# Kernel tuning notes

Hardware: AMD Instinct MI355X
Metric: run time of the kernel (lower is better)

Reference implementation:

```python
import jax, jax.numpy as jnp
import numpy as np

N_EMBED = 1024
N_HEADS = 16
HEAD_DIM = N_EMBED // N_HEADS


def setup_inputs() -> dict:
    key = jax.random.key(0)
    ks = jax.random.split(key, 5)
    x = jax.random.normal(ks[0], (4, 2048, N_EMBED), dtype=jnp.float32)
    # Linear params stored as [in, out] (y = x @ W + b), math-equivalent to torch Linear
    scale_attn = 1.0 / np.sqrt(N_EMBED)
    W_attn = jax.random.normal(ks[1], (N_EMBED, 3 * N_EMBED), dtype=jnp.float32) * scale_attn
    b_attn = jax.random.normal(ks[2], (3 * N_EMBED,), dtype=jnp.float32) * 0.02
    W_proj = jax.random.normal(ks[3], (N_EMBED, N_EMBED), dtype=jnp.float32) * scale_attn
    b_proj = jax.random.normal(ks[4], (N_EMBED,), dtype=jnp.float32) * 0.02
    return {"x": x, "W_attn": W_attn, "b_attn": b_attn, "W_proj": W_proj, "b_proj": b_proj}


def reference(x, W_attn, b_attn, W_proj, b_proj):
    BS, SL, ED = x.shape
    qkv = x @ W_attn + b_attn                      # [B, S, 3E]
    q, k, v = jnp.split(qkv, 3, axis=2)
    # [B, H, S, D]
    def heads(t):
        return t.reshape(BS, SL, N_HEADS, HEAD_DIM).transpose(0, 2, 1, 3)
    q, k, v = heads(q), heads(k), heads(v)
    att = jnp.einsum('bhqd,bhkd->bhqk', q, k) * (HEAD_DIM ** -0.5)
    causal = jnp.tril(jnp.ones((SL, SL), dtype=bool))
    att = jnp.where(causal[None, None], att, -jnp.inf)
    att = jax.nn.softmax(att, axis=-1)
    y = jnp.einsum('bhqk,bhkd->bhqd', att, v)      # [B, H, S, D]
    y = y.transpose(0, 2, 1, 3).reshape(BS, SL, ED)
    return y @ W_proj + b_proj
```

## Files before the change

### kernel.cpp

```cpp
#include <hip/hip_runtime.h>


#define BATCH 4
#define SEQ   2048
#define EMB   1024
#define NH    16
#define HD    64

typedef __bf16 bf16;
typedef __bf16 bf16x8 __attribute__((ext_vector_type(8)));
typedef float  f32x4  __attribute__((ext_vector_type(4)));

__device__ __forceinline__ void ld_lds16(const void* g, void* l) {
  __builtin_amdgcn_global_load_lds(
      (const __attribute__((address_space(1))) void*)g,
      (__attribute__((address_space(3))) void*)l, 16, 0, 0);
}

__global__ void cvt_f32_bf16(const float* __restrict__ in, bf16* __restrict__ out, int n) {
  int i = (blockIdx.x * blockDim.x + threadIdx.x) * 4;
  if (i + 3 < n) {
    float4 v = *(const float4*)(in + i);
    bf16 o0 = (bf16)v.x, o1 = (bf16)v.y, o2 = (bf16)v.z, o3 = (bf16)v.w;
    out[i] = o0; out[i+1] = o1; out[i+2] = o2; out[i+3] = o3;
  }
}

__global__ void transpose_cvt2(const float* __restrict__ Wa, const float* __restrict__ Wp,
                               bf16* __restrict__ WaT, bf16* __restrict__ WpT) {
  __shared__ float tile[32][33];
  int bx = blockIdx.x;
  const float* W; bf16* WT; int N;
  if (bx < 96) { W = Wa; WT = WaT; N = 3072; }
  else         { W = Wp; WT = WpT; N = 1024; bx -= 96; }
  int n0 = bx * 32, k0 = blockIdx.y * 32;
  int tx = threadIdx.x & 31, ty = threadIdx.x >> 5;
#pragma unroll
  for (int r = 0; r < 4; r++) {
    int k = k0 + ty + r * 8;
    tile[ty + r * 8][tx] = W[(long)k * N + n0 + tx];
  }
  __syncthreads();
#pragma unroll
  for (int r = 0; r < 4; r++) {
    int n = n0 + ty + r * 8;
    WT[(long)n * EMB + k0 + tx] = (bf16)tile[tx][ty + r * 8];
  }
}

#define QSCALE 0.18033688f

template <int BNT>
__global__ __launch_bounds__(256, 3) void gemm_bt(
    const bf16* __restrict__ A, const bf16* __restrict__ Bt,
    const float* __restrict__ bias, int Kdim, int Ncols, int mode,
    bf16* __restrict__ q, bf16* __restrict__ k, bf16* __restrict__ v,
    float* __restrict__ out)
{
  constexpr int NF = BNT / 32;
  __shared__ __align__(16) bf16 Al[128 * 64];
  __shared__ __align__(16) bf16 Bl[BNT * 64];
  int lin = blockIdx.x;
  int xcd = lin & 7, s = lin >> 3;
  int bx = s >> 3, by = xcd * 8 + (s & 7);
  int m0 = by * 128;
  int n0 = bx * BNT;
  int t = threadIdx.x;
  int wave = t >> 6, lane = t & 63;
  int l15 = lane & 15, quad = lane >> 4;
  int wm = (wave & 1) * 64, wn = (wave >> 1) * (BNT / 2);

  f32x4 acc[4][NF] = {};

  for (int kt = 0; kt < Kdim; kt += 64) {
    __syncthreads();
#pragma unroll
    for (int it = 0; it < 4; ++it) {
      int c = it * 256 + t;
      int row = c >> 3, u = c & 7;
      ld_lds16(&A[(long)(m0 + row) * Kdim + kt + ((u ^ (row & 7)) * 8)],
               &Al[(it * 256 + wave * 64) * 8]);
    }
#pragma unroll
    for (int it = 0; it < BNT / 32; ++it) {
      int c = it * 256 + t;
      int row = c >> 3, u = c & 7;
      ld_lds16(&Bt[(long)(n0 + row) * Kdim + kt + ((u ^ (row & 7)) * 8)],
               &Bl[(it * 256 + wave * 64) * 8]);
    }
    __syncthreads();
#pragma unroll
    for (int ks = 0; ks < 2; ++ks) {
      bf16x8 af[4], bfr[NF];
#pragma unroll
      for (int i = 0; i < 4; ++i) {
        int r = wm + i * 16 + l15;
        af[i] = *(const bf16x8*)(&Al[r * 64 + (((ks * 4 + quad) ^ (r & 7)) * 8)]);
      }
#pragma unroll
      for (int i = 0; i < NF; ++i) {
        int r = wn + i * 16 + l15;
        bfr[i] = *(const bf16x8*)(&Bl[r * 64 + (((ks * 4 + quad) ^ (r & 7)) * 8)]);
      }
#pragma unroll
      for (int mi = 0; mi < 4; ++mi)
#pragma unroll
        for (int ni = 0; ni < NF; ++ni)
          acc[mi][ni] = __builtin_amdgcn_mfma_f32_16x16x32_bf16(af[mi], bfr[ni], acc[mi][ni], 0, 0, 0);
    }
  }

#pragma unroll
  for (int mi = 0; mi < 4; ++mi) {
#pragma unroll
    for (int ni = 0; ni < NF; ++ni) {
      int gcol = n0 + wn + ni * 16 + l15;
      float bv = bias[gcol];
#pragma unroll
      for (int i = 0; i < 4; ++i) {
        int grow = m0 + wm + mi * 16 + quad * 4 + i;
        float val = acc[mi][ni][i] + bv;
        if (mode == 0) {
          int which = gcol >> 10, e = gcol & 1023;
          int h = e >> 6, d = e & 63;
          int b = grow >> 11, ss = grow & 2047;
          if (which == 0) {
            q[(((long)b * NH + h) * SEQ + ss) * HD + d] = (bf16)(val * QSCALE);
          } else if (which == 1) {
            k[(((long)b * NH + h) * SEQ + ss) * HD + d] = (bf16)val;
          } else {
            v[(((long)b * NH + h) * HD + d) * SEQ + ss] = (bf16)val;
          }
        } else {
          out[(long)grow * Ncols + gcol] = val;
        }
      }
    }
  }
}

#define LDP 72

__global__ __launch_bounds__(256, 2) void attn(
    const bf16* __restrict__ Q, const bf16* __restrict__ K,
    const bf16* __restrict__ Vt, bf16* __restrict__ Y)
{
  __shared__ __align__(16) bf16 Kl[64 * 64];
  __shared__ __align__(16) bf16 Vl[64 * 64];
  __shared__ __align__(16) bf16 Pl[4][32 * LDP];
  int L = blockIdx.x;
  int a = L >> 3;
  int hd = (L & 7) + 8 * (a & 7);
  int st = a >> 3;
  int b = hd >> 4, h = hd & 15;
  const bf16* Qp  = Q  + (((long)b * NH + h) * SEQ) * HD;
  const bf16* Kp  = K  + (((long)b * NH + h) * SEQ) * HD;
  const bf16* Vtp = Vt + (((long)b * NH + h) * HD) * SEQ;
  int t = threadIdx.x, wave = t >> 6, lane = t & 63;
  int l15 = lane & 15, quad = lane >> 4;

#pragma unroll 1
  for (int pass = 0; pass < 2; ++pass) {
    int q0 = (pass == 0) ? st * 128 : (SEQ - 128) - st * 128;
    int wq0 = q0 + wave * 32;

    bf16x8 qf[2][2];
#pragma unroll
    for (int m = 0; m < 2; ++m) {
      const bf16* qrow = Qp + (long)(wq0 + m * 16 + l15) * HD + quad * 8;
      qf[m][0] = *(const bf16x8*)(qrow);
      qf[m][1] = *(const bf16x8*)(qrow + 32);
    }
    float lrow[2][4] = {};
    f32x4 oacc[2][4] = {};

    int ntiles = q0 / 64 + 2;
#pragma unroll 1
    for (int kt = 0; kt < ntiles; ++kt) {
      int k0 = kt * 64;
      __syncthreads();
#pragma unroll
      for (int it = 0; it < 2; ++it) {
        int cu = it * 256 + t;
        int row = cu >> 3, u = cu & 7;
        ld_lds16(&Kp[(long)(k0 + row) * HD + ((u ^ (row & 7)) * 8)],
                 &Kl[(it * 256 + wave * 64) * 8]);
        ld_lds16(&Vtp[(long)row * SEQ + k0 + ((u ^ (row & 7)) * 8)],
                 &Vl[(it * 256 + wave * 64) * 8]);
      }
      __syncthreads();
      if (k0 > wq0 + 31) continue;

      f32x4 sc[2][4] = {};
#pragma unroll
      for (int kk = 0; kk < 2; ++kk) {
#pragma unroll
        for (int ni = 0; ni < 4; ++ni) {
          int r = ni * 16 + l15, u = kk * 4 + quad;
          bf16x8 kfr = *(const bf16x8*)(&Kl[r * 64 + ((u ^ (r & 7)) * 8)]);
          sc[0][ni] = __builtin_amdgcn_mfma_f32_16x16x32_bf16(qf[0][kk], kfr, sc[0][ni], 0, 0, 0);
          sc[1][ni] = __builtin_amdgcn_mfma_f32_16x16x32_bf16(qf[1][kk], kfr, sc[1][ni], 0, 0, 0);
        }
      }

      bool full = (k0 + 63 <= wq0);
#pragma unroll
      for (int m = 0; m < 2; ++m) {
#pragma unroll
        for (int i = 0; i < 4; ++i) {
          int qr = wq0 + m * 16 + quad * 4 + i;
          float e[4];
#pragma unroll
          for (int ni = 0; ni < 4; ++ni) {
            float x = sc[m][ni][i];
            if (!full) x = (k0 + ni * 16 + l15 <= qr) ? x : -1e30f;
            e[ni] = __builtin_amdgcn_exp2f(x);
          }
          lrow[m][i] += (e[0] + e[1]) + (e[2] + e[3]);
          int prow = (m * 16 + quad * 4 + i) * LDP;
#pragma unroll
          for (int ni = 0; ni < 4; ++ni)
            Pl[wave][prow + ni * 16 + l15] = (bf16)e[ni];
        }
      }
      asm volatile("s_waitcnt lgkmcnt(0)" ::: "memory");
#pragma unroll
      for (int kk = 0; kk < 2; ++kk) {
        int kbase = kk * 32 + quad * 8;
        bf16x8 pf0 = *(const bf16x8*)(&Pl[wave][(l15) * LDP + kbase]);
        bf16x8 pf1 = *(const bf16x8*)(&Pl[wave][(16 + l15) * LDP + kbase]);
#pragma unroll
        for (int ni = 0; ni < 4; ++ni) {
          int dd = ni * 16 + l15, u = kk * 4 + quad;
          bf16x8 vf = *(const bf16x8*)(&Vl[dd * 64 + ((u ^ (dd & 7)) * 8)]);
          oacc[0][ni] = __builtin_amdgcn_mfma_f32_16x16x32_bf16(pf0, vf, oacc[0][ni], 0, 0, 0);
          oacc[1][ni] = __builtin_amdgcn_mfma_f32_16x16x32_bf16(pf1, vf, oacc[1][ni], 0, 0, 0);
        }
      }
    }
#pragma unroll
    for (int m = 0; m < 2; ++m) {
#pragma unroll
      for (int i = 0; i < 4; ++i) {
        float rs = lrow[m][i];
#pragma unroll
        for (int off = 8; off; off >>= 1) rs += __shfl_xor(rs, off, 16);
        float inv = 1.0f / rs;
        int qr = wq0 + m * 16 + quad * 4 + i;
        bf16* dst = Y + ((long)(b * SEQ + qr)) * EMB + h * HD;
#pragma unroll
        for (int ni = 0; ni < 4; ++ni)
          dst[ni * 16 + l15] = (bf16)(oacc[m][ni][i] * inv);
      }
    }
  }
}

extern "C" void kernel_launch(void* const* d_in, const int* in_sizes, int n_in,
                              void* d_out, int out_size, void* d_ws, size_t ws_size,
                              hipStream_t stream) {
  const float* x      = (const float*)d_in[0];
  const float* W_attn = (const float*)d_in[1];
  const float* b_attn = (const float*)d_in[2];
  const float* W_proj = (const float*)d_in[3];
  const float* b_proj = (const float*)d_in[4];
  float* out = (float*)d_out;
  char* ws = (char*)d_ws;
  bf16* xb  = (bf16*)(ws);
  bf16* WaT = (bf16*)(ws + 16777216);
  bf16* WpT = (bf16*)(ws + 23068672);
  bf16* Qb  = (bf16*)(ws + 25165824);
  bf16* Kb  = (bf16*)(ws + 41943040);
  bf16* Vtb = (bf16*)(ws + 58720256);
  bf16* Yb  = (bf16*)(ws + 75497472);

  cvt_f32_bf16<<<8192, 256, 0, stream>>>(x, xb, BATCH * SEQ * EMB);
  transpose_cvt2<<<dim3(128, 32), 256, 0, stream>>>(W_attn, W_proj, WaT, WpT);
  gemm_bt<128><<<1536, 256, 0, stream>>>(xb, WaT, b_attn, EMB, 3 * EMB, 0,
                                         Qb, Kb, Vtb, nullptr);
  attn<<<512, 256, 0, stream>>>(Qb, Kb, Vtb, Yb);
  gemm_bt<64><<<1024, 256, 0, stream>>>(Yb, WpT, b_proj, EMB, EMB, 1,
                                        nullptr, nullptr, nullptr, out);
}
```

Before: 248.6 us.

## Replace GEMM with 8-wave 256-row tiled kernel using double-buffered LDS pipeline

Replaces the 4-wave 128-row GEMM with an 8-wave, 256-row-tile kernel. It double-buffers LDS with global-to-LDS loads issued ahead, splits the MFMA work into halves interleaved with barriers and priority bumps, and uses a K step of 32 with an XOR swizzle. The epilogue is specialized per output (Q/K, V, or the projection output) through template parameters. This aims to overlap memory loads with MFMA and raise data reuse per tile, at the cost of higher register pressure and fewer blocks.

```diff
diff --git a/kernel.cpp b/kernel.cpp
--- a/kernel.cpp
+++ b/kernel.cpp
@@ -50,93 +50,151 @@
 
 #define QSCALE 0.18033688f
 
-template <int BNT>
-__global__ __launch_bounds__(256, 3) void gemm_bt(
+template <int MODE, int NF>
+__global__ __launch_bounds__(512, 2) void gemm8p(
     const bf16* __restrict__ A, const bf16* __restrict__ Bt,
-    const float* __restrict__ bias, int Kdim, int Ncols, int mode,
+    const float* __restrict__ bias,
     bf16* __restrict__ q, bf16* __restrict__ k, bf16* __restrict__ v,
     float* __restrict__ out)
 {
-  constexpr int NF = BNT / 32;
-  __shared__ __align__(16) bf16 Al[128 * 64];
-  __shared__ __align__(16) bf16 Bl[BNT * 64];
+  constexpr int BN = NF * 64;
+  constexpr int WN = NF * 16;
+  constexpr int BELEM = BN * 32;
+  __shared__ __align__(16) bf16 lds[16384 + 2 * BELEM];
   int lin = blockIdx.x;
   int xcd = lin & 7, s = lin >> 3;
-  int bx = s >> 3, by = xcd * 8 + (s & 7);
-  int m0 = by * 128;
-  int n0 = bx * BNT;
+  int by = xcd * 4 + (s & 3);
+  int bx = s >> 2;
+  int m0 = by * 256, n0 = bx * BN;
   int t = threadIdx.x;
-  int wave = t >> 6, lane = t & 63;
+  int wid = t >> 6, lane = t & 63;
   int l15 = lane & 15, quad = lane >> 4;
-  int wm = (wave & 1) * 64, wn = (wave >> 1) * (BNT / 2);
-
-  f32x4 acc[4][NF] = {};
-
-  for (int kt = 0; kt < Kdim; kt += 64) {
-    __syncthreads();
-#pragma unroll
-    for (int it = 0; it < 4; ++it) {
-      int c = it * 256 + t;
-      int row = c >> 3, u = c & 7;
-      ld_lds16(&A[(long)(m0 + row) * Kdim + kt + ((u ^ (row & 7)) * 8)],
-               &Al[(it * 256 + wave * 64) * 8]);
+  int wr = wid >> 2, wc = wid & 3;
+
+  const bf16* Ag = A + (long)m0 * EMB;
+  const bf16* Bg = Bt + (long)n0 * EMB;
+
+  f32x4 acc[8][NF] = {};
+  bf16x8 af[8], bfr[NF];
+  constexpr int NT = EMB / 32;
+
+#define LDSA(b) (lds + (b) * 8192)
+#define LDSB(b) (lds + 16384 + (b) * BELEM)
+
+#define ISSUE128(gbase, rowoff, ldst, ktt)                                     \
+  { int r_ = (rowoff) + (t >> 2);                                              \
+    ld_lds16(&(gbase)[(long)r_ * EMB + (ktt) + (((t & 3) ^ (r_ & 3)) * 8)],    \
+             (ldst) + ((rowoff) + wid * 16) * 32); }
+
+#define RD_A(mi) { int r_ = wr * 128 + (mi) * 16 + l15;                        \
+    af[mi] = *(const bf16x8*)&Ab[r_ * 32 + ((quad ^ (r_ & 3)) * 8)]; }
+#define RD_B(ni) { int r_ = wc * WN + (ni) * 16 + l15;                         \
+    bfr[ni] = *(const bf16x8*)&Bb[r_ * 32 + ((quad ^ (r_ & 3)) * 8)]; }
+
+#define FENCE asm volatile("" ::: "memory")
+#define BAR   { FENCE; __builtin_amdgcn_s_barrier(); FENCE; }
+
+#define MFMAC(nlo)                                                             \
+  { __builtin_amdgcn_s_setprio(1);                                             \
+    _Pragma("unroll") for (int mi_ = 0; mi_ < 8; ++mi_)                        \
+      _Pragma("unroll") for (int nj_ = 0; nj_ < NF / 2; ++nj_)                 \
+        acc[mi_][(nlo) + nj_] = __builtin_amdgcn_mfma_f32_16x16x32_bf16(       \
+            af[mi_], bfr[(nlo) + nj_], acc[mi_][(nlo) + nj_], 0, 0, 0);        \
+    __builtin_amdgcn_s_setprio(0); }
+
+  ISSUE128(Ag, 0,   LDSA(0), 0);
+  ISSUE128(Ag, 128, LDSA(0), 0);
+  ISSUE128(Bg, 0,   LDSB(0), 0);
+  if constexpr (NF == 4) ISSUE128(Bg, 128, LDSB(0), 0);
+  ISSUE128(Ag, 0,   LDSA(1), 32);
+  asm volatile("s_waitcnt vmcnt(1)" ::: "memory");
+  BAR;
+
+#pragma unroll 2
+  for (int tt = 0; tt < NT; ++tt) {
+    const bf16* Ab = LDSA(tt & 1);
+    const bf16* Bb = LDSB(tt & 1);
+    bf16* An = LDSA((tt + 1) & 1);
+    bf16* Bn = LDSB((tt + 1) & 1);
+    bf16* Ac = LDSA(tt & 1);
+    int kn  = (tt + 1 < NT ? tt + 1 : NT - 1) * 32;
+    int kn2 = (tt + 2 < NT ? tt + 2 : NT - 1) * 32;
+
+#pragma unroll
+    for (int mi = 0; mi < 8; ++mi) RD_A(mi);
+#pragma unroll
+    for (int ni = 0; ni < NF / 2; ++ni) RD_B(ni);
+    ISSUE128(Ag, 128, An, kn);
+    ISSUE128(Bg, 0,   Bn, kn);
+    if constexpr (NF == 4) ISSUE128(Bg, 128, Bn, kn);
+    BAR; MFMAC(0); BAR;
+#pragma unroll
+    for (int ni = NF / 2; ni < NF; ++ni) RD_B(ni);
+    ISSUE128(Ag, 0, Ac, kn2);
+    asm volatile("s_waitcnt vmcnt(1)" ::: "memory");
+    BAR; MFMAC(NF / 2); BAR;
+  }
+
+  asm volatile("s_waitcnt vmcnt(0)" ::: "memory");
+  __syncthreads();
+
+  if (MODE == 1) {
+#pragma unroll
+    for (int mi = 0; mi < 8; ++mi)
+#pragma unroll
+      for (int ni = 0; ni < NF; ++ni) {
+        int gcol = n0 + wc * WN + ni * 16 + l15;
+        float bv = bias[gcol];
+#pragma unroll
+        for (int i = 0; i < 4; ++i) {
+          int grow = m0 + wr * 128 + mi * 16 + quad * 4 + i;
+          out[(long)grow * EMB + gcol] = acc[mi][ni][i] + bv;
+        }
+      }
+  } else {
+    int which = n0 >> 10;
+    if (which < 2) {
+      bf16* dst = (which == 0) ? q : k;
+      float scale = (which == 0) ? QSCALE : 1.0f;
+#pragma unroll
+      for (int mi = 0; mi < 8; ++mi)
+#pragma unroll
+        for (int ni = 0; ni < NF; ++ni) {
+          int gcol = n0 + wc * WN + ni * 16 + l15;
+          float bv = bias[gcol];
+          int e = gcol & 1023, h = e >> 6, d = e & 63;
+#pragma unroll
+          for (int i = 0; i < 4; ++i) {
+            int grow = m0 + wr * 128 + mi * 16 + quad * 4 + i;
+            int b = grow >> 11, ss = grow & 2047;
+            dst[(((long)b * NH + h) * SEQ + ss) * HD + d] =
+                (bf16)((acc[mi][ni][i] + bv) * scale);
+          }
+        }
+    } else {
+#pragma unroll
+      for (int mi = 0; mi < 8; ++mi)
+#pragma unroll
+        for (int ni = 0; ni < NF; ++ni) {
+          int gcol = n0 + wc * WN + ni * 16 + l15;
+          float bv = bias[gcol];
+          int e = gcol & 1023, h = e >> 6, d = e & 63;
+#pragma unroll
+          for (int i = 0; i < 4; ++i) {
+            int grow = m0 + wr * 128 + mi * 16 + quad * 4 + i;
+            int b = grow >> 11, ss = grow & 2047;
+            v[(((long)b * NH + h) * HD + d) * SEQ + ss] =
+                (bf16)(acc[mi][ni][i] + bv);
+          }
+        }
     }
-#pragma unroll
-    for (int it = 0; it < BNT / 32; ++it) {
-      int c = it * 256 + t;
-      int row = c >> 3, u = c & 7;
-      ld_lds16(&Bt[(long)(n0 + row) * Kdim + kt + ((u ^ (row & 7)) * 8)],
-               &Bl[(it * 256 + wave * 64) * 8]);
-    }
-    __syncthreads();
-#pragma unroll
-    for (int ks = 0; ks < 2; ++ks) {
-      bf16x8 af[4], bfr[NF];
-#pragma unroll
-      for (int i = 0; i < 4; ++i) {
-        int r = wm + i * 16 + l15;
-        af[i] = *(const bf16x8*)(&Al[r * 64 + (((ks * 4 + quad) ^ (r & 7)) * 8)]);
-      }
-#pragma unroll
-      for (int i = 0; i < NF; ++i) {
-        int r = wn + i * 16 + l15;
-        bfr[i] = *(const bf16x8*)(&Bl[r * 64 + (((ks * 4 + quad) ^ (r & 7)) * 8)]);
-      }
-#pragma unroll
-      for (int mi = 0; mi < 4; ++mi)
-#pragma unroll
-        for (int ni = 0; ni < NF; ++ni)
-          acc[mi][ni] = __builtin_amdgcn_mfma_f32_16x16x32_bf16(af[mi], bfr[ni], acc[mi][ni], 0, 0, 0);
-    }
-  }
-
-#pragma unroll
-  for (int mi = 0; mi < 4; ++mi) {
-#pragma unroll
-    for (int ni = 0; ni < NF; ++ni) {
-      int gcol = n0 + wn + ni * 16 + l15;
-      float bv = bias[gcol];
-#pragma unroll
-      for (int i = 0; i < 4; ++i) {
-        int grow = m0 + wm + mi * 16 + quad * 4 + i;
-        float val = acc[mi][ni][i] + bv;
-        if (mode == 0) {
-          int which = gcol >> 10, e = gcol & 1023;
-          int h = e >> 6, d = e & 63;
-          int b = grow >> 11, ss = grow & 2047;
-          if (which == 0) {
-            q[(((long)b * NH + h) * SEQ + ss) * HD + d] = (bf16)(val * QSCALE);
-          } else if (which == 1) {
-            k[(((long)b * NH + h) * SEQ + ss) * HD + d] = (bf16)val;
-          } else {
-            v[(((long)b * NH + h) * HD + d) * SEQ + ss] = (bf16)val;
-          }
-        } else {
-          out[(long)grow * Ncols + gcol] = val;
-        }
-      }
-    }
-  }
+  }
+#undef LDSA
+#undef LDSB
+#undef ISSUE128
+#undef RD_A
+#undef RD_B
+#undef MFMAC
 }
 
 #define LDP 72
@@ -276,9 +334,8 @@
 
   cvt_f32_bf16<<<8192, 256, 0, stream>>>(x, xb, BATCH * SEQ * EMB);
   transpose_cvt2<<<dim3(128, 32), 256, 0, stream>>>(W_attn, W_proj, WaT, WpT);
-  gemm_bt<128><<<1536, 256, 0, stream>>>(xb, WaT, b_attn, EMB, 3 * EMB, 0,
-                                         Qb, Kb, Vtb, nullptr);
+  gemm8p<0, 4><<<384, 512, 0, stream>>>(xb, WaT, b_attn, Qb, Kb, Vtb, nullptr);
   attn<<<512, 256, 0, stream>>>(Qb, Kb, Vtb, Yb);
-  gemm_bt<64><<<1024, 256, 0, stream>>>(Yb, WpT, b_proj, EMB, EMB, 1,
+  gemm8p<1, 2><<<256, 512, 0, stream>>>(Yb, WpT, b_proj,
                                         nullptr, nullptr, nullptr, out);
 }
```

Result: slower. 271.3 us (+9.1%).
